# Kernel optimization log

Hardware: AMD Instinct MI355X
Metric: run time of the kernel (lower is better)

Reference implementation:

```python
import jax, jax.numpy as jnp
import numpy as np

D_K = 64  # per-head dim, used as softmax scale (matches __init__ d_k)

def setup_inputs() -> dict:
    key = jax.random.key(0)
    kq, kk, kv, km = jax.random.split(key, 4)
    B, H, S, D = 2, 16, 2048, D_K
    q = jax.random.normal(kq, (B, H, S, D), dtype=jnp.float32)
    k = jax.random.normal(kk, (B, H, S, D), dtype=jnp.float32)
    v = jax.random.normal(kv, (B, H, S, D), dtype=jnp.float32)
    mask = jax.random.randint(km, (B, 1, S, S), 0, 2).astype(jnp.bool_)
    return {"q": q, "k": k, "v": v, "mask": mask}

def reference(q, k, v, mask):
    # attn = (q / sqrt(d_k)) @ k^T  -> [B,H,S,S]
    scale = 1.0 / jnp.sqrt(jnp.float32(D_K))
    attn = jnp.einsum("bhqd,bhkd->bhqk", q * scale, k)
    # faithful to torch masked_fill(mask, -1e-09) -- note tiny value, not -1e9
    attn = jnp.where(mask, jnp.float32(-1e-9), attn)
    weights = jax.nn.softmax(attn, axis=-1)  # dropout p=0.0 -> identity
    output = jnp.einsum("bhqk,bhkd->bhqd", weights, v)
    return (output, weights)
```

## Files before the change

kernel.cpp:

```cpp
#include <hip/hip_runtime.h>
#include <hip/hip_bf16.h>


namespace {

constexpr int kS = 2048;
constexpr int kD = 64;
constexpr int kBH = 32;
constexpr int kTQW = 16;
constexpr int kNW = 4;
constexpr int kTQB = kTQW * kNW;
constexpr int kChunk = 64;
constexpr int kNC = kS / kChunk;
constexpr int kNB = kBH * (kS / kTQB);
constexpr size_t kWOff = (size_t)kBH * kS * kD;

typedef __attribute__((ext_vector_type(8))) short bf16x8;
typedef __attribute__((ext_vector_type(4))) float f32x4;

__device__ inline short f2bf(float f) {
  union { float f; unsigned u; } x; x.f = f;
  return (short)((x.u + 0x7fffu + ((x.u >> 16) & 1u)) >> 16);
}

__device__ inline bf16x8 cvt8(float4 a, float4 b, float scale) {
  bf16x8 f;
  f[0] = f2bf(a.x * scale); f[1] = f2bf(a.y * scale);
  f[2] = f2bf(a.z * scale); f[3] = f2bf(a.w * scale);
  f[4] = f2bf(b.x * scale); f[5] = f2bf(b.y * scale);
  f[6] = f2bf(b.z * scale); f[7] = f2bf(b.w * scale);
  return f;
}

__global__ __launch_bounds__(256, 4) void attn_fused(
    const float* __restrict__ qg, const float* __restrict__ kg,
    const float* __restrict__ vg, const unsigned int* __restrict__ mg,
    float* __restrict__ outg) {
  __shared__ __align__(16) short Kt[kChunk][72];
  __shared__ __align__(16) short Vt[kD][72];
  __shared__ __align__(16) short Wt[kNW][kTQW][72];
  __shared__ __align__(16) unsigned char Msk[kChunk][80];

  const int tid  = threadIdx.x;
  const int wv   = tid >> 6;
  const int lane = tid & 63;
  const int l15  = lane & 15;
  const int quad = lane >> 4;

  const int bid  = blockIdx.x;
  const int work = ((bid & 7) << 7) | (bid >> 3);
  const int qt   = work & 31;
  const int bh   = work >> 5;
  const int b    = bh >> 4;
  const int q0b  = qt * kTQB;

  int allW32 = 1, allI32 = 1, allBF = 1;
#pragma unroll
  for (int i = 0; i < 64; ++i) {
    const unsigned u = mg[i];
    const unsigned lo = u & 0xFFFFu, hi = u >> 16;
    allW32 &= (int)(u == 0u || u == 0x3F800000u);
    allI32 &= (int)(u == 0u || u == 1u);
    allBF  &= (int)((lo == 0u || lo == 0x3F80u) && (hi == 0u || hi == 0x3F80u));
  }
  int msz;
  if (allI32)      msz = 4;
  else if (allW32) msz = 4;
  else if (allBF)  msz = 2;
  else             msz = 1;
  const unsigned char* mB = (const unsigned char*)mg + (size_t)b * kS * kS * msz;

  const float* qbase = qg + (size_t)bh * kS * kD;
  const float* kbase = kg + (size_t)bh * kS * kD;
  const float* vbase = vg + (size_t)bh * kS * kD;
  float* obase = outg + (size_t)bh * kS * kD;
  float* wbase = outg + kWOff + (size_t)bh * kS * kS;

  bf16x8 aq[2];
#pragma unroll
  for (int dh = 0; dh < 2; ++dh) {
    const float* p = qbase + (size_t)(q0b + wv * kTQW + l15) * kD + dh * 32 + quad * 8;
    aq[dh] = cvt8(*(const float4*)p, *(const float4*)(p + 4), 0.125f);
  }

  const int si = tid >> 2;
  const int sj = (tid & 3) << 4;
  const int vd = (tid & 7) << 3;
  const int vk = (tid >> 3) << 1;

  float4 rk[4], rv[4];
  uint4 rmq;

  auto k_issue = [&](int k0) {
    const float* p = kbase + (size_t)(k0 + si) * kD + sj;
    rk[0] = ((const float4*)p)[0];
    rk[1] = *(const float4*)(p + 4);
    rk[2] = *(const float4*)(p + 8);
    rk[3] = *(const float4*)(p + 12);
  };
  auto k_write = [&]() {
    *(bf16x8*)&Kt[si][sj]     = cvt8(rk[0], rk[1], 1.0f);
    *(bf16x8*)&Kt[si][sj + 8] = cvt8(rk[2], rk[3], 1.0f);
  };

  auto v_issue = [&](int k0) {
    const float* p = vbase + (size_t)(k0 + vk) * kD + vd;
    rv[0] = ((const float4*)p)[0];
    rv[1] = *(const float4*)(p + 4);
    rv[2] = *(const float4*)(p + kD);
    rv[3] = *(const float4*)(p + kD + 4);
  };
  auto v_write = [&]() {
    const float* lo = (const float*)&rv[0];
    const float* hi = (const float*)&rv[2];
#pragma unroll
    for (int d = 0; d < 8; ++d) {
      const int dd = vd + d;
      const int ps = (vk >> 1) ^ (((dd >> 3) & 7) << 2);
      const unsigned u = (unsigned)(unsigned short)f2bf(lo[d]) |
                         ((unsigned)(unsigned short)f2bf(hi[d]) << 16);
      *(unsigned*)&Vt[dd][2 * ps] = u;
    }
  };

  auto m_issue = [&](int k0) {
    if (msz == 1)
      rmq = *(const uint4*)(mB + (size_t)(q0b + si) * kS + (size_t)(k0 + sj));
  };
  auto m_write = [&](int k0) {
    if (msz == 1) {
      *(uint4*)&Msk[si][sj] = rmq;
    } else if (msz == 4) {
      const size_t eoff = (size_t)(q0b + si) * kS + (size_t)(k0 + sj);
      const unsigned int* p = (const unsigned int*)mB + eoff;
      unsigned int* dst = (unsigned int*)&Msk[si][sj];
#pragma unroll
      for (int g = 0; g < 4; ++g) {
        uint4 e = *(const uint4*)(p + 4 * g);
        dst[g] = (e.x ? 1u : 0u) | ((e.y ? 1u : 0u) << 8) |
                 ((e.z ? 1u : 0u) << 16) | ((e.w ? 1u : 0u) << 24);
      }
    } else {
      const size_t eoff = (size_t)(q0b + si) * kS + (size_t)(k0 + sj);
      const unsigned int* p = (const unsigned int*)((const unsigned short*)mB + eoff);
      unsigned int* dst = (unsigned int*)&Msk[si][sj];
#pragma unroll
      for (int g = 0; g < 4; ++g) {
        const unsigned int a = p[2 * g], c = p[2 * g + 1];
        dst[g] = ((a & 0xFFFFu) ? 1u : 0u) | (((a >> 16) ? 1u : 0u) << 8) |
                 (((c & 0xFFFFu) ? 1u : 0u) << 16) | (((c >> 16) ? 1u : 0u) << 24);
      }
    }
  };

  float lsum[4] = {0.f, 0.f, 0.f, 0.f};
  k_issue(0);
  m_issue(0);
  for (int c = 0; c < kNC; ++c) {
    const int k0 = c * kChunk;
    __syncthreads();
    k_write();
    m_write(k0);
    if (c + 1 < kNC) { k_issue(k0 + kChunk); m_issue(k0 + kChunk); }
    __syncthreads();
#pragma unroll
    for (int cg = 0; cg < 4; ++cg) {
      bf16x8 bk0 = *(const bf16x8*)&Kt[cg * 16 + l15][quad * 8];
      bf16x8 bk1 = *(const bf16x8*)&Kt[cg * 16 + l15][32 + quad * 8];
      f32x4 acc = {0.f, 0.f, 0.f, 0.f};
      acc = __builtin_amdgcn_mfma_f32_16x16x32_bf16(aq[0], bk0, acc, 0, 0, 0);
      acc = __builtin_amdgcn_mfma_f32_16x16x32_bf16(aq[1], bk1, acc, 0, 0, 0);
#pragma unroll
      for (int r = 0; r < 4; ++r) {
        const int lrow = wv * kTQW + quad * 4 + r;
        const float e = __expf(acc[r]);
        lsum[r] += (Msk[lrow][cg * 16 + l15] != 0) ? 1.0f : e;
      }
    }
  }

  k_issue(0);
  v_issue(0);
  m_issue(0);

  float inv_l[4];
#pragma unroll
  for (int r = 0; r < 4; ++r) {
    float t = lsum[r];
    t += __shfl_xor(t, 1, 16);
    t += __shfl_xor(t, 2, 16);
    t += __shfl_xor(t, 4, 16);
    t += __shfl_xor(t, 8, 16);
    inv_l[r] = 1.0f / t;
  }

  f32x4 acco[4];
#pragma unroll
  for (int d = 0; d < 4; ++d) acco[d] = (f32x4){0.f, 0.f, 0.f, 0.f};

  for (int c = 0; c < kNC; ++c) {
    const int k0 = c * kChunk;
    __syncthreads();
    k_write();
    v_write();
    m_write(k0);
    if (c + 1 < kNC) { k_issue(k0 + kChunk); v_issue(k0 + kChunk); m_issue(k0 + kChunk); }
    __syncthreads();
#pragma unroll
    for (int cg = 0; cg < 4; ++cg) {
      bf16x8 bk0 = *(const bf16x8*)&Kt[cg * 16 + l15][quad * 8];
      bf16x8 bk1 = *(const bf16x8*)&Kt[cg * 16 + l15][32 + quad * 8];
      f32x4 acc = {0.f, 0.f, 0.f, 0.f};
      acc = __builtin_amdgcn_mfma_f32_16x16x32_bf16(aq[0], bk0, acc, 0, 0, 0);
      acc = __builtin_amdgcn_mfma_f32_16x16x32_bf16(aq[1], bk1, acc, 0, 0, 0);
      const int kcol = k0 + cg * 16 + l15;
#pragma unroll
      for (int r = 0; r < 4; ++r) {
        const int lrow = wv * kTQW + quad * 4 + r;
        const float e = __expf(acc[r]);
        const float w = ((Msk[lrow][cg * 16 + l15] != 0) ? 1.0f : e) * inv_l[r];
        __builtin_nontemporal_store(w, &wbase[(size_t)(q0b + lrow) * kS + kcol]);
        Wt[wv][quad * 4 + r][cg * 16 + l15] = f2bf(w);
      }
    }
#pragma unroll
    for (int ks = 0; ks < 2; ++ks) {
      bf16x8 aw = *(const bf16x8*)&Wt[wv][l15][ks * 32 + quad * 8];
#pragma unroll
      for (int d = 0; d < 4; ++d) {
        const int dd = d * 16 + l15;
        const int psb = (ks * 16 + quad * 4) ^ (((dd >> 3) & 7) << 2);
        bf16x8 bv = *(const bf16x8*)&Vt[dd][2 * psb];
        acco[d] = __builtin_amdgcn_mfma_f32_16x16x32_bf16(aw, bv, acco[d], 0, 0, 0);
      }
    }
  }

#pragma unroll
  for (int d = 0; d < 4; ++d)
#pragma unroll
    for (int r = 0; r < 4; ++r)
      __builtin_nontemporal_store(
          acco[d][r],
          &obase[(size_t)(q0b + wv * kTQW + quad * 4 + r) * kD + d * 16 + l15]);
}

}

extern "C" void kernel_launch(void* const* d_in, const int* in_sizes, int n_in,
                              void* d_out, int out_size, void* d_ws, size_t ws_size,
                              hipStream_t stream) {
  const float* q = (const float*)d_in[0];
  const float* k = (const float*)d_in[1];
  const float* v = (const float*)d_in[2];
  const unsigned int* mask = (const unsigned int*)d_in[3];
  float* out = (float*)d_out;
  attn_fused<<<dim3(kNB), dim3(256), 0, stream>>>(q, k, v, mask, out);
}
```

Measured before the change: 790.9 us.

## Load K fragments directly to registers, double-buffer V/mask, transpose MFMA outputs

Removes the K shared-memory staging: each wave loads its K fragments straight from global into registers, with two tiles in flight. V and mask tiles are double-buffered in LDS, so each chunk needs one barrier instead of two. The MFMA operands are swapped so each lane holds four consecutive key columns of one query row. This allows vectorized float4 nontemporal stores of weights and output, plus a single-scalar row-sum reduction. The cost is redundant K global loads per wave (the four waves each fetch the same K) and higher register pressure.

```diff
diff --git a/kernel.cpp b/kernel.cpp
--- a/kernel.cpp
+++ b/kernel.cpp
@@ -12,15 +12,21 @@
 constexpr int kTQB = kTQW * kNW;
 constexpr int kChunk = 64;
 constexpr int kNC = kS / kChunk;
+constexpr int kNT = kNC * 4;
 constexpr int kNB = kBH * (kS / kTQB);
 constexpr size_t kWOff = (size_t)kBH * kS * kD;
 
 typedef __attribute__((ext_vector_type(8))) short bf16x8;
 typedef __attribute__((ext_vector_type(4))) float f32x4;
+typedef __attribute__((ext_vector_type(2))) unsigned u32x2;
 
 __device__ inline short f2bf(float f) {
   union { float f; unsigned u; } x; x.f = f;
   return (short)((x.u + 0x7fffu + ((x.u >> 16) & 1u)) >> 16);
+}
+
+__device__ inline unsigned pk2bf(float a, float b) {
+  return (unsigned)(unsigned short)f2bf(a) | ((unsigned)(unsigned short)f2bf(b) << 16);
 }
 
 __device__ inline bf16x8 cvt8(float4 a, float4 b, float scale) {
@@ -32,14 +38,19 @@
   return f;
 }
 
+__device__ inline void block_sync_lds() {
+  asm volatile("s_waitcnt lgkmcnt(0)" ::: "memory");
+  __builtin_amdgcn_s_barrier();
+  asm volatile("" ::: "memory");
+}
+
 __global__ __launch_bounds__(256, 4) void attn_fused(
     const float* __restrict__ qg, const float* __restrict__ kg,
     const float* __restrict__ vg, const unsigned int* __restrict__ mg,
     float* __restrict__ outg) {
-  __shared__ __align__(16) short Kt[kChunk][72];
-  __shared__ __align__(16) short Vt[kD][72];
+  __shared__ __align__(16) short Vt[2][kD][72];
+  __shared__ __align__(16) unsigned char Msk[2][kTQB][80];
   __shared__ __align__(16) short Wt[kNW][kTQW][72];
-  __shared__ __align__(16) unsigned char Msk[kChunk][80];
 
   const int tid  = threadIdx.x;
   const int wv   = tid >> 6;
@@ -76,41 +87,40 @@
   float* obase = outg + (size_t)bh * kS * kD;
   float* wbase = outg + kWOff + (size_t)bh * kS * kS;
 
+  const int qrow = q0b + wv * kTQW + l15;
+
   bf16x8 aq[2];
 #pragma unroll
   for (int dh = 0; dh < 2; ++dh) {
-    const float* p = qbase + (size_t)(q0b + wv * kTQW + l15) * kD + dh * 32 + quad * 8;
+    const float* p = qbase + (size_t)qrow * kD + dh * 32 + quad * 8;
     aq[dh] = cvt8(*(const float4*)p, *(const float4*)(p + 4), 0.125f);
   }
+
+  float4 kb0[4], kb1[4];
+  auto k_issue0 = [&](int tt) {
+    const float* p = kbase + (size_t)(tt * 16 + l15) * kD + quad * 8;
+    kb0[0] = *(const float4*)p;        kb0[1] = *(const float4*)(p + 4);
+    kb0[2] = *(const float4*)(p + 32); kb0[3] = *(const float4*)(p + 36);
+  };
+  auto k_issue1 = [&](int tt) {
+    const float* p = kbase + (size_t)(tt * 16 + l15) * kD + quad * 8;
+    kb1[0] = *(const float4*)p;        kb1[1] = *(const float4*)(p + 4);
+    kb1[2] = *(const float4*)(p + 32); kb1[3] = *(const float4*)(p + 36);
+  };
 
   const int si = tid >> 2;
   const int sj = (tid & 3) << 4;
   const int vd = (tid & 7) << 3;
   const int vk = (tid >> 3) << 1;
-
-  float4 rk[4], rv[4];
+  float4 rv[4];
   uint4 rmq;
 
-  auto k_issue = [&](int k0) {
-    const float* p = kbase + (size_t)(k0 + si) * kD + sj;
-    rk[0] = ((const float4*)p)[0];
-    rk[1] = *(const float4*)(p + 4);
-    rk[2] = *(const float4*)(p + 8);
-    rk[3] = *(const float4*)(p + 12);
-  };
-  auto k_write = [&]() {
-    *(bf16x8*)&Kt[si][sj]     = cvt8(rk[0], rk[1], 1.0f);
-    *(bf16x8*)&Kt[si][sj + 8] = cvt8(rk[2], rk[3], 1.0f);
-  };
-
-  auto v_issue = [&](int k0) {
-    const float* p = vbase + (size_t)(k0 + vk) * kD + vd;
-    rv[0] = ((const float4*)p)[0];
-    rv[1] = *(const float4*)(p + 4);
-    rv[2] = *(const float4*)(p + kD);
-    rv[3] = *(const float4*)(p + kD + 4);
-  };
-  auto v_write = [&]() {
+  auto v_issue = [&](int c) {
+    const float* p = vbase + (size_t)(c * kChunk + vk) * kD + vd;
+    rv[0] = *(const float4*)p;        rv[1] = *(const float4*)(p + 4);
+    rv[2] = *(const float4*)(p + kD); rv[3] = *(const float4*)(p + kD + 4);
+  };
+  auto v_write = [&](int buf) {
     const float* lo = (const float*)&rv[0];
     const float* hi = (const float*)&rv[2];
 #pragma unroll
@@ -119,21 +129,21 @@
       const int ps = (vk >> 1) ^ (((dd >> 3) & 7) << 2);
       const unsigned u = (unsigned)(unsigned short)f2bf(lo[d]) |
                          ((unsigned)(unsigned short)f2bf(hi[d]) << 16);
-      *(unsigned*)&Vt[dd][2 * ps] = u;
-    }
-  };
-
-  auto m_issue = [&](int k0) {
+      *(unsigned*)&Vt[buf][dd][2 * ps] = u;
+    }
+  };
+
+  auto m_issue = [&](int c) {
     if (msz == 1)
-      rmq = *(const uint4*)(mB + (size_t)(q0b + si) * kS + (size_t)(k0 + sj));
-  };
-  auto m_write = [&](int k0) {
+      rmq = *(const uint4*)(mB + (size_t)(q0b + si) * kS + (size_t)(c * kChunk + sj));
+  };
+  auto m_write = [&](int buf, int c) {
     if (msz == 1) {
-      *(uint4*)&Msk[si][sj] = rmq;
+      *(uint4*)&Msk[buf][si][sj] = rmq;
     } else if (msz == 4) {
-      const size_t eoff = (size_t)(q0b + si) * kS + (size_t)(k0 + sj);
+      const size_t eoff = (size_t)(q0b + si) * kS + (size_t)(c * kChunk + sj);
       const unsigned int* p = (const unsigned int*)mB + eoff;
-      unsigned int* dst = (unsigned int*)&Msk[si][sj];
+      unsigned int* dst = (unsigned int*)&Msk[buf][si][sj];
 #pragma unroll
       for (int g = 0; g < 4; ++g) {
         uint4 e = *(const uint4*)(p + 4 * g);
@@ -141,108 +151,110 @@
                  ((e.z ? 1u : 0u) << 16) | ((e.w ? 1u : 0u) << 24);
       }
     } else {
-      const size_t eoff = (size_t)(q0b + si) * kS + (size_t)(k0 + sj);
+      const size_t eoff = (size_t)(q0b + si) * kS + (size_t)(c * kChunk + sj);
       const unsigned int* p = (const unsigned int*)((const unsigned short*)mB + eoff);
-      unsigned int* dst = (unsigned int*)&Msk[si][sj];
+      unsigned int* dst = (unsigned int*)&Msk[buf][si][sj];
 #pragma unroll
       for (int g = 0; g < 4; ++g) {
-        const unsigned int a = p[2 * g], c = p[2 * g + 1];
+        const unsigned int a = p[2 * g], cc = p[2 * g + 1];
         dst[g] = ((a & 0xFFFFu) ? 1u : 0u) | (((a >> 16) ? 1u : 0u) << 8) |
-                 (((c & 0xFFFFu) ? 1u : 0u) << 16) | (((c >> 16) ? 1u : 0u) << 24);
-      }
-    }
-  };
-
-  float lsum[4] = {0.f, 0.f, 0.f, 0.f};
-  k_issue(0);
+                 (((cc & 0xFFFFu) ? 1u : 0u) << 16) | (((cc >> 16) ? 1u : 0u) << 24);
+      }
+    }
+  };
+
+  const int mrow = wv * kTQW + l15;
+
+  float lsum = 0.f;
   m_issue(0);
+  k_issue0(0); k_issue1(1);
+  m_write(0, 0);
+  m_issue(1);
+  block_sync_lds();
+  int p = 0;
   for (int c = 0; c < kNC; ++c) {
-    const int k0 = c * kChunk;
-    __syncthreads();
-    k_write();
-    m_write(k0);
-    if (c + 1 < kNC) { k_issue(k0 + kChunk); m_issue(k0 + kChunk); }
-    __syncthreads();
-#pragma unroll
-    for (int cg = 0; cg < 4; ++cg) {
-      bf16x8 bk0 = *(const bf16x8*)&Kt[cg * 16 + l15][quad * 8];
-      bf16x8 bk1 = *(const bf16x8*)&Kt[cg * 16 + l15][32 + quad * 8];
+    if (c + 1 < kNC) m_write(p ^ 1, c + 1);
+    if (c + 2 < kNC) m_issue(c + 2);
+#pragma unroll
+    for (int t = 0; t < 4; ++t) {
+      bf16x8 f0, f1;
+      if ((t & 1) == 0) { f0 = cvt8(kb0[0], kb0[1], 1.f); f1 = cvt8(kb0[2], kb0[3], 1.f); }
+      else              { f0 = cvt8(kb1[0], kb1[1], 1.f); f1 = cvt8(kb1[2], kb1[3], 1.f); }
+      const int nt_ = c * 4 + t + 2;
+      if (nt_ < kNT) { if (t & 1) k_issue1(nt_); else k_issue0(nt_); }
       f32x4 acc = {0.f, 0.f, 0.f, 0.f};
-      acc = __builtin_amdgcn_mfma_f32_16x16x32_bf16(aq[0], bk0, acc, 0, 0, 0);
-      acc = __builtin_amdgcn_mfma_f32_16x16x32_bf16(aq[1], bk1, acc, 0, 0, 0);
+      acc = __builtin_amdgcn_mfma_f32_16x16x32_bf16(f0, aq[0], acc, 0, 0, 0);
+      acc = __builtin_amdgcn_mfma_f32_16x16x32_bf16(f1, aq[1], acc, 0, 0, 0);
+      const unsigned mu = *(const unsigned*)&Msk[p][mrow][t * 16 + quad * 4];
 #pragma unroll
       for (int r = 0; r < 4; ++r) {
-        const int lrow = wv * kTQW + quad * 4 + r;
         const float e = __expf(acc[r]);
-        lsum[r] += (Msk[lrow][cg * 16 + l15] != 0) ? 1.0f : e;
-      }
-    }
-  }
-
-  k_issue(0);
-  v_issue(0);
-  m_issue(0);
-
-  float inv_l[4];
-#pragma unroll
-  for (int r = 0; r < 4; ++r) {
-    float t = lsum[r];
-    t += __shfl_xor(t, 1, 16);
-    t += __shfl_xor(t, 2, 16);
-    t += __shfl_xor(t, 4, 16);
-    t += __shfl_xor(t, 8, 16);
-    inv_l[r] = 1.0f / t;
-  }
+        lsum += ((mu >> (8 * r)) & 0xFFu) ? 1.0f : e;
+      }
+    }
+    block_sync_lds();
+    p ^= 1;
+  }
+
+  lsum += __shfl_xor(lsum, 16);
+  lsum += __shfl_xor(lsum, 32);
+  const float inv = 1.0f / lsum;
 
   f32x4 acco[4];
 #pragma unroll
   for (int d = 0; d < 4; ++d) acco[d] = (f32x4){0.f, 0.f, 0.f, 0.f};
 
+  v_issue(0); m_issue(0);
+  k_issue0(0); k_issue1(1);
+  v_write(0); m_write(0, 0);
+  v_issue(1); m_issue(1);
+  block_sync_lds();
+  p = 0;
+  float* const wrow = wbase + (size_t)qrow * kS;
+  const int swz = (l15 & 7) << 3;
   for (int c = 0; c < kNC; ++c) {
-    const int k0 = c * kChunk;
-    __syncthreads();
-    k_write();
-    v_write();
-    m_write(k0);
-    if (c + 1 < kNC) { k_issue(k0 + kChunk); v_issue(k0 + kChunk); m_issue(k0 + kChunk); }
-    __syncthreads();
-#pragma unroll
-    for (int cg = 0; cg < 4; ++cg) {
-      bf16x8 bk0 = *(const bf16x8*)&Kt[cg * 16 + l15][quad * 8];
-      bf16x8 bk1 = *(const bf16x8*)&Kt[cg * 16 + l15][32 + quad * 8];
+    if (c + 1 < kNC) { v_write(p ^ 1); m_write(p ^ 1, c + 1); }
+    if (c + 2 < kNC) { v_issue(c + 2); m_issue(c + 2); }
+#pragma unroll
+    for (int t = 0; t < 4; ++t) {
+      bf16x8 f0, f1;
+      if ((t & 1) == 0) { f0 = cvt8(kb0[0], kb0[1], 1.f); f1 = cvt8(kb0[2], kb0[3], 1.f); }
+      else              { f0 = cvt8(kb1[0], kb1[1], 1.f); f1 = cvt8(kb1[2], kb1[3], 1.f); }
+      const int nt_ = c * 4 + t + 2;
+      if (nt_ < kNT) { if (t & 1) k_issue1(nt_); else k_issue0(nt_); }
       f32x4 acc = {0.f, 0.f, 0.f, 0.f};
-      acc = __builtin_amdgcn_mfma_f32_16x16x32_bf16(aq[0], bk0, acc, 0, 0, 0);
-      acc = __builtin_amdgcn_mfma_f32_16x16x32_bf16(aq[1], bk1, acc, 0, 0, 0);
-      const int kcol = k0 + cg * 16 + l15;
-#pragma unroll
-      for (int r = 0; r < 4; ++r) {
-        const int lrow = wv * kTQW + quad * 4 + r;
-        const float e = __expf(acc[r]);
-        const float w = ((Msk[lrow][cg * 16 + l15] != 0) ? 1.0f : e) * inv_l[r];
-        __builtin_nontemporal_store(w, &wbase[(size_t)(q0b + lrow) * kS + kcol]);
-        Wt[wv][quad * 4 + r][cg * 16 + l15] = f2bf(w);
-      }
+      acc = __builtin_amdgcn_mfma_f32_16x16x32_bf16(f0, aq[0], acc, 0, 0, 0);
+      acc = __builtin_amdgcn_mfma_f32_16x16x32_bf16(f1, aq[1], acc, 0, 0, 0);
+      const unsigned mu = *(const unsigned*)&Msk[p][mrow][t * 16 + quad * 4];
+      const float w0 = ((mu       & 0xFFu) ? 1.0f : __expf(acc[0])) * inv;
+      const float w1 = ((mu >> 8  & 0xFFu) ? 1.0f : __expf(acc[1])) * inv;
+      const float w2 = ((mu >> 16 & 0xFFu) ? 1.0f : __expf(acc[2])) * inv;
+      const float w3 = ((mu >> 24        ) ? 1.0f : __expf(acc[3])) * inv;
+      u32x2 uu = {pk2bf(w0, w1), pk2bf(w2, w3)};
+      *(u32x2*)&Wt[wv][l15][(t * 16 + quad * 4) ^ swz] = uu;
+      f32x4 wq = {w0, w1, w2, w3};
+      __builtin_nontemporal_store(wq, (f32x4*)(wrow + c * kChunk + t * 16 + quad * 4));
     }
 #pragma unroll
     for (int ks = 0; ks < 2; ++ks) {
-      bf16x8 aw = *(const bf16x8*)&Wt[wv][l15][ks * 32 + quad * 8];
-#pragma unroll
-      for (int d = 0; d < 4; ++d) {
-        const int dd = d * 16 + l15;
+      bf16x8 aw = *(const bf16x8*)&Wt[wv][l15][(ks * 32 + quad * 8) ^ swz];
+#pragma unroll
+      for (int dt = 0; dt < 4; ++dt) {
+        const int dd = dt * 16 + l15;
         const int psb = (ks * 16 + quad * 4) ^ (((dd >> 3) & 7) << 2);
-        bf16x8 bv = *(const bf16x8*)&Vt[dd][2 * psb];
-        acco[d] = __builtin_amdgcn_mfma_f32_16x16x32_bf16(aw, bv, acco[d], 0, 0, 0);
-      }
-    }
-  }
-
-#pragma unroll
-  for (int d = 0; d < 4; ++d)
-#pragma unroll
-    for (int r = 0; r < 4; ++r)
-      __builtin_nontemporal_store(
-          acco[d][r],
-          &obase[(size_t)(q0b + wv * kTQW + quad * 4 + r) * kD + d * 16 + l15]);
+        bf16x8 bv = *(const bf16x8*)&Vt[p][dd][2 * psb];
+        acco[dt] = __builtin_amdgcn_mfma_f32_16x16x32_bf16(bv, aw, acco[dt], 0, 0, 0);
+      }
+    }
+    block_sync_lds();
+    p ^= 1;
+  }
+
+#pragma unroll
+  for (int dt = 0; dt < 4; ++dt) {
+    f32x4 o = acco[dt];
+    __builtin_nontemporal_store(o, (f32x4*)(obase + (size_t)qrow * kD + dt * 16 + quad * 4));
+  }
 }
 
 }
```

Result: slower. 1.114 ms (+40.9%).
